# Kernel tuning notes

Measured on AMD Instinct MI355X. Metric: run time of the kernel, lower is better.

Reference implementation:

```python
import jax, jax.numpy as jnp
import numpy as np

N = 100000   # nodes (single 'paper' node type)
E = 1600000  # edges per relation
R = 3        # relation types
IN_DIM, HID_DIM, OUT_DIM = 128, 128, 64


def setup_inputs() -> dict:
    key = jax.random.key(0)
    ks = jax.random.split(key, 5)
    x = jax.random.normal(ks[0], (N, IN_DIM), dtype=jnp.float32)
    edges = jax.random.randint(ks[1], (R, 2, E), 0, N, dtype=jnp.int32)  # [rel, (src,dst), E]
    W1 = jax.random.normal(ks[2], (R, IN_DIM, HID_DIM), dtype=jnp.float32) * 0.05
    b1 = jnp.zeros((R, HID_DIM), dtype=jnp.float32)
    W2 = jax.random.normal(ks[3], (R, HID_DIM, OUT_DIM), dtype=jnp.float32) * 0.05
    b2 = jnp.zeros((R, OUT_DIM), dtype=jnp.float32)
    return {"x": x, "edges": edges, "W1": W1, "b1": b1, "W2": W2, "b2": b2}


def _hetero_gcn_layer(x, edges, W, b):
    """Per-relation DGL GraphConv (norm='both') summed across relations.
    y = sum_r  D_in_r^{-1/2} A_r^T (D_out_r^{-1/2} x) W_r + b_r
    """
    n = x.shape[0]
    ones = jnp.ones((edges.shape[-1],), x.dtype)
    out = jnp.zeros((n, W.shape[-1]), x.dtype)
    for r in range(edges.shape[0]):  # small fixed relation count
        src, dst = edges[r, 0], edges[r, 1]
        deg_out = jnp.maximum(jax.ops.segment_sum(ones, src, num_segments=n), 1.0)
        deg_in = jnp.maximum(jax.ops.segment_sum(ones, dst, num_segments=n), 1.0)
        # apply weight before aggregation (linear, math-equivalent; smaller msgs when out<=in)
        m = (x * (deg_out ** -0.5)[:, None]) @ W[r]          # [N, out]
        agg = jax.ops.segment_sum(m[src], dst, num_segments=n)  # gather+scatter SpMM
        out = out + agg * (deg_in ** -0.5)[:, None] + b[r]
    return out


def reference(x, edges, W1, b1, W2, b2):
    h = jax.nn.relu(_hetero_gcn_layer(x, edges, W1, b1))
    return _hetero_gcn_layer(h, edges, W2, b2)
```

## Files before the change

kernel.cpp:

```cpp
#include <hip/hip_runtime.h>

#define NODES 100000
#define NEDGE 1600000
#define NREL  3
#define DIN   128
#define DHID  128
#define DOUT  64

#define NBUCK 782
#define CHUNK 6144
#define NBLK  261
#define SEGCAP 8192

typedef unsigned short ushort_t;
typedef __attribute__((ext_vector_type(8))) short bf16x8;
typedef __attribute__((ext_vector_type(4))) float f32x4;

__device__ __forceinline__ unsigned f2bf1(float f) {
    unsigned u = __float_as_uint(f);
    return (u + 0x7fffu + ((u >> 16) & 1u)) >> 16;
}

__device__ __forceinline__ void scan_nbuck(unsigned* hist, unsigned* loff,
                                           unsigned* wred, int tid) {
    const int lane = tid & 63, wid = tid >> 6;
    unsigned s4[4];
    unsigned tsum = 0;
    const int sbase = tid * 4;
#pragma unroll
    for (int j = 0; j < 4; j++) {
        const unsigned c = (sbase + j < NBUCK) ? hist[sbase + j] : 0u;
        s4[j] = tsum;
        tsum += c;
    }
    unsigned incl = tsum;
    for (int o = 1; o < 64; o <<= 1) {
        const unsigned t = __shfl_up(incl, o, 64);
        if (lane >= o) incl += t;
    }
    if (lane == 63) wred[wid] = incl;
    __syncthreads();
    if (tid == 0) {
        unsigned a = 0;
        for (int w = 0; w < 4; w++) { const unsigned t = wred[w]; wred[w] = a; a += t; }
    }
    __syncthreads();
    const unsigned texcl = wred[wid] + incl - tsum;
#pragma unroll
    for (int j = 0; j < 4; j++)
        if (sbase + j < NBUCK) loff[sbase + j] = texcl + s4[j];
    __syncthreads();
}

__global__ __launch_bounds__(256) void partition_dst_kernel(
    const int* __restrict__ edges, int* __restrict__ bcur,
    unsigned* __restrict__ inter32) {
    __shared__ unsigned hist[NBUCK];
    __shared__ unsigned loff[NBUCK];
    __shared__ unsigned resv[NBUCK];
    __shared__ unsigned sorted[CHUNK];
    __shared__ ushort_t bof[CHUNK];
    __shared__ unsigned wred[4];
    const int tid = threadIdx.x;
    const int r = blockIdx.y;
    const int e0 = blockIdx.x * CHUNK;
    const int e1 = min(e0 + CHUNK, NEDGE);
    const int len = e1 - e0;
    const int* __restrict__ src = edges + (size_t)r * 2 * NEDGE;
    const int* __restrict__ dst = src + NEDGE;

    for (int i = tid; i < NBUCK; i += 256) hist[i] = 0;
    __syncthreads();
    for (int e = e0 + tid; e < e1; e += 256)
        atomicAdd(&hist[dst[e] >> 7], 1u);
    __syncthreads();
    scan_nbuck(hist, loff, wred, tid);
    for (int i = tid; i < NBUCK; i += 256) {
        const unsigned c = hist[i];
        resv[i] = c ? (unsigned)atomicAdd(&bcur[i], (int)c) : 0u;
        hist[i] = 0;
    }
    __syncthreads();
    for (int e = e0 + tid; e < e1; e += 256) {
        const int d = dst[e];
        const int b = d >> 7;
        const unsigned rank = atomicAdd(&hist[b], 1u);
        const unsigned pos = loff[b] + rank;
        sorted[pos] = ((unsigned)(d & 127) << 19) | (unsigned)(r * NODES + src[e]);
        bof[pos] = (ushort_t)b;
    }
    __syncthreads();
    for (int i = tid; i < len; i += 256) {
        const int b = bof[i];
        inter32[(size_t)b * SEGCAP + resv[b] + ((unsigned)i - loff[b])] = sorted[i];
    }
}

__global__ __launch_bounds__(256) void partition_src_kernel(
    const int* __restrict__ edges, int* __restrict__ bcur,
    ushort_t* __restrict__ inter16) {
    __shared__ unsigned hist[NBUCK];
    __shared__ unsigned loff[NBUCK];
    __shared__ unsigned resv[NBUCK];
    __shared__ unsigned sorted[CHUNK];
    __shared__ unsigned wred[4];
    const int tid = threadIdx.x;
    const int r = blockIdx.y;
    const int e0 = blockIdx.x * CHUNK;
    const int e1 = min(e0 + CHUNK, NEDGE);
    const int len = e1 - e0;
    const int* __restrict__ src = edges + (size_t)r * 2 * NEDGE;

    for (int i = tid; i < NBUCK; i += 256) hist[i] = 0;
    __syncthreads();
    for (int e = e0 + tid; e < e1; e += 256)
        atomicAdd(&hist[src[e] >> 7], 1u);
    __syncthreads();
    scan_nbuck(hist, loff, wred, tid);
    for (int i = tid; i < NBUCK; i += 256) {
        const unsigned c = hist[i];
        resv[i] = c ? (unsigned)atomicAdd(&bcur[i], (int)c) : 0u;
        hist[i] = 0;
    }
    __syncthreads();
    for (int e = e0 + tid; e < e1; e += 256) {
        const int s = src[e];
        const int b = s >> 7;
        const unsigned rank = atomicAdd(&hist[b], 1u);
        sorted[loff[b] + rank] =
            ((unsigned)b << 9) | ((unsigned)r << 7) | (unsigned)(s & 127);
    }
    __syncthreads();
    for (int i = tid; i < len; i += 256) {
        const unsigned w = sorted[i];
        const int b = w >> 9;
        inter16[(size_t)b * SEGCAP + resv[b] + ((unsigned)i - loff[b])] =
            (ushort_t)(w & 0x1ffu);
    }
}

__global__ __launch_bounds__(1024) void bscan_kernel(
    const int* __restrict__ bcur, int* __restrict__ bucketBase) {
    __shared__ int wsum[16];
    const int tid = threadIdx.x, lane = tid & 63, wid = tid >> 6;
    const int v = (tid < NBUCK) ? bcur[tid] : 0;
    int incl = v;
    for (int off = 1; off < 64; off <<= 1) {
        const int t = __shfl_up(incl, off, 64);
        if (lane >= off) incl += t;
    }
    if (lane == 63) wsum[wid] = incl;
    __syncthreads();
    if (tid == 0) {
        int a = 0;
        for (int w = 0; w < 16; w++) { const int t = wsum[w]; wsum[w] = a; a += t; }
    }
    __syncthreads();
    const int excl = wsum[wid] + incl - v;
    if (tid <= NBUCK) bucketBase[tid] = excl;
}

__global__ __launch_bounds__(256) void build_deg_kernel(
    const ushort_t* __restrict__ inter16, const int* __restrict__ bcur2,
    float* __restrict__ rout) {
    __shared__ int degR[NREL][128];
    const int b = blockIdx.x;
    const int tid = threadIdx.x;
    const int len = bcur2[b];
    const ushort_t* __restrict__ seg = inter16 + (size_t)b * SEGCAP;
    for (int i = tid; i < NREL * 128; i += 256) ((int*)degR)[i] = 0;
    __syncthreads();
    for (int s = tid; s < len; s += 256) {
        const unsigned p = seg[s];
        atomicAdd(&degR[p >> 7][p & 127], 1);
    }
    __syncthreads();
    const int n0 = b << 7;
    if (tid < 128) {
        const int node = n0 + tid;
        if (node < NODES) {
#pragma unroll
            for (int r = 0; r < NREL; r++) {
                const int d = degR[r][tid];
                rout[r * NODES + node] = rsqrtf((float)(d ? d : 1));
            }
        }
    }
}

__global__ __launch_bounds__(256) void build_kernel(
    const unsigned* __restrict__ inter, const int* __restrict__ bucketBase,
    int* __restrict__ csr, int* __restrict__ rowptr, unsigned* __restrict__ rel01,
    float* __restrict__ rin) {
    __shared__ int degR[NREL][128];
    __shared__ int rp[129];
    __shared__ int cur3[NREL][128];
    __shared__ int csr_lds[SEGCAP];
    const int b = blockIdx.x;
    const int tid = threadIdx.x;
    const int n0 = b << 7;
    const int nn = min(128, NODES - n0);
    const int s0 = bucketBase[b], s1 = bucketBase[b + 1];
    const int len = s1 - s0;
    const unsigned* __restrict__ seg = inter + (size_t)b * SEGCAP;
    for (int i = tid; i < NREL * 128; i += 256) ((int*)degR)[i] = 0;
    __syncthreads();
    for (int s = tid; s < len; s += 256) {
        const unsigned w = seg[s];
        const int dl = w >> 19;
        const int p = (int)(w & 0x7FFFFu);
        const int rel = p < NODES ? 0 : (p < 2 * NODES ? 1 : 2);
        atomicAdd(&degR[rel][dl], 1);
    }
    __syncthreads();
    if (tid == 0) {
        int a = 0;
        for (int i = 0; i < 128; i++) {
            rp[i] = a;
            a += degR[0][i] + degR[1][i] + degR[2][i];
        }
        rp[128] = a;
    }
    __syncthreads();
    if (tid < 128) {
        const int c0 = rp[tid];
        cur3[0][tid] = c0;
        cur3[1][tid] = c0 + degR[0][tid];
        cur3[2][tid] = c0 + degR[0][tid] + degR[1][tid];
    }
    if (tid < nn) {
        const int node = n0 + tid;
        rowptr[node] = s0 + rp[tid];
        rel01[node] = (unsigned)degR[0][tid] | ((unsigned)degR[1][tid] << 16);
#pragma unroll
        for (int r = 0; r < NREL; r++) {
            const int d = degR[r][tid];
            rin[r * NODES + node] = rsqrtf((float)(d ? d : 1));
        }
    }
    if (b == NBUCK - 1 && tid == 0) rowptr[NODES] = s1;
    __syncthreads();
    for (int s = tid; s < len; s += 256) {
        const unsigned w = seg[s];
        const int dl = w >> 19;
        const int p = (int)(w & 0x7FFFFu);
        const int rel = p < NODES ? 0 : (p < 2 * NODES ? 1 : 2);
        const int srcn = p - rel * NODES;
        const int slot = atomicAdd(&cur3[rel][dl], 1);
        csr_lds[slot] = srcn;
    }
    __syncthreads();
    for (int i = tid; i < len; i += 256) csr[s0 + i] = csr_lds[i];
}

__global__ __launch_bounds__(256) void tobf_kernel(const float* __restrict__ x,
                                                   ushort_t* __restrict__ xb) {
    const size_t i = ((size_t)blockIdx.x * 256 + threadIdx.x) * 8;
    const float4 a = *(const float4*)(x + i);
    const float4 b = *(const float4*)(x + i + 4);
    uint4 p;
    p.x = f2bf1(a.x) | (f2bf1(a.y) << 16);
    p.y = f2bf1(a.z) | (f2bf1(a.w) << 16);
    p.z = f2bf1(b.x) | (f2bf1(b.y) << 16);
    p.w = f2bf1(b.z) | (f2bf1(b.w) << 16);
    *(uint4*)(xb + i) = p;
}

template <int ODIM>
__global__ __launch_bounds__(256) void mfma_gemm(
    const ushort_t* __restrict__ A, const float* __restrict__ rout_all,
    const float* __restrict__ W_all, ushort_t* __restrict__ m_all) {
    constexpr int PAD = DIN + 8;
    constexpr int NT = ODIM / 16;
    __shared__ ushort_t Al[64 * PAD];
    __shared__ ushort_t Wt[ODIM * PAD];
    const int tid = threadIdx.x;
    const int rel = blockIdx.y;
    const int row0 = blockIdx.x * 64;
    const float* __restrict__ rout = rout_all + (size_t)rel * NODES;
    const float* __restrict__ W = W_all + (size_t)rel * DIN * ODIM;
    ushort_t* __restrict__ mout = m_all + (size_t)rel * NODES * ODIM;

    for (int idx = tid * 8; idx < 64 * DIN; idx += 2048) {
        const int rr = idx >> 7;
        const int kk = idx & 127;
        const int row = row0 + rr;
        uint4 p = make_uint4(0u, 0u, 0u, 0u);
        if (row < NODES) p = *(const uint4*)(A + (size_t)row * DIN + kk);
        *(uint4*)(Al + rr * PAD + kk) = p;
    }
    for (int idx = tid; idx < ODIM * (DIN / 8); idx += 256) {
        const int c = idx % ODIM;
        const int kh = idx / ODIM;
        unsigned pk[4];
#pragma unroll
        for (int j = 0; j < 4; j++) {
            const float lo = W[(size_t)(kh * 8 + 2 * j) * ODIM + c];
            const float hi = W[(size_t)(kh * 8 + 2 * j + 1) * ODIM + c];
            pk[j] = f2bf1(lo) | (f2bf1(hi) << 16);
        }
        *(uint4*)(Wt + c * PAD + kh * 8) = *(const uint4*)pk;
    }
    __syncthreads();

    const int l = tid & 63;
    const int wv = tid >> 6;
    const int lr = l & 15;
    const int lg = l >> 4;
    f32x4 acc[NT];
#pragma unroll
    for (int j = 0; j < NT; j++) acc[j] = (f32x4){0.f, 0.f, 0.f, 0.f};

    const ushort_t* ap = Al + (wv * 16 + lr) * PAD + lg * 8;
    const ushort_t* bp = Wt + lr * PAD + lg * 8;
#pragma unroll
    for (int ks = 0; ks < DIN; ks += 32) {
        const bf16x8 af = *(const bf16x8*)(ap + ks);
#pragma unroll
        for (int j = 0; j < NT; j++) {
            const bf16x8 bfr = *(const bf16x8*)(bp + (size_t)j * 16 * PAD + ks);
            acc[j] = __builtin_amdgcn_mfma_f32_16x16x32_bf16(af, bfr, acc[j], 0, 0, 0);
        }
    }

    const int orow0 = row0 + wv * 16 + lg * 4;
#pragma unroll
    for (int r = 0; r < 4; r++) {
        const int row = orow0 + r;
        if (row < NODES) {
            const float sc = rout[row];
#pragma unroll
            for (int j = 0; j < NT; j++)
                mout[(size_t)row * ODIM + j * 16 + lr] =
                    (ushort_t)f2bf1(acc[j][r] * sc);
        }
    }
}

template <int ODIM, bool L1>
__global__ __launch_bounds__(256) void agg_kernel(
    const ushort_t* __restrict__ m_all, const int* __restrict__ rowptr,
    const unsigned* __restrict__ rel01, const int* __restrict__ csr,
    const float* __restrict__ rin, const float* __restrict__ bias,
    float* __restrict__ outf, ushort_t* __restrict__ outh) {
    constexpr int CPT = ODIM / 16;
    const int v = blockIdx.x * 16 + (threadIdx.x >> 4);
    const int colbase = (threadIdx.x & 15) * CPT;
    const int b = rowptr[v];
    const int e2 = rowptr[v + 1];
    const unsigned c01 = rel01[v];
    const int cnt0 = (int)(c01 & 0xffffu);
    const int cnt1 = (int)(c01 >> 16);

    float acc[CPT];
#pragma unroll
    for (int j = 0; j < CPT; j++) acc[j] = 0.f;

    const ushort_t* mr = m_all + colbase;
    int beg = b;
#pragma unroll
    for (int r = 0; r < NREL; r++) {
        const int end = (r == 0) ? b + cnt0 : (r == 1) ? b + cnt0 + cnt1 : e2;
        float s[CPT];
#pragma unroll
        for (int j = 0; j < CPT; j++) s[j] = 0.f;
#pragma unroll 4
        for (int i = beg; i < end; i++) {
            const unsigned off = (unsigned)csr[i] * ODIM;
            if constexpr (CPT == 8) {
                const uint4 p = *(const uint4*)(mr + off);
                s[0] += __uint_as_float(p.x << 16);
                s[1] += __uint_as_float(p.x & 0xffff0000u);
                s[2] += __uint_as_float(p.y << 16);
                s[3] += __uint_as_float(p.y & 0xffff0000u);
                s[4] += __uint_as_float(p.z << 16);
                s[5] += __uint_as_float(p.z & 0xffff0000u);
                s[6] += __uint_as_float(p.w << 16);
                s[7] += __uint_as_float(p.w & 0xffff0000u);
            } else {
                const uint2 p = *(const uint2*)(mr + off);
                s[0] += __uint_as_float(p.x << 16);
                s[1] += __uint_as_float(p.x & 0xffff0000u);
                s[2] += __uint_as_float(p.y << 16);
                s[3] += __uint_as_float(p.y & 0xffff0000u);
            }
        }
        const float sc = rin[r * NODES + v];
#pragma unroll
        for (int j = 0; j < CPT; j++) acc[j] = fmaf(s[j], sc, acc[j]);
        beg = end;
        mr += (size_t)NODES * ODIM;
    }

    if (L1) {
        unsigned pk[CPT / 2];
#pragma unroll
        for (int j = 0; j < CPT; j += 2) {
            const int c0 = colbase + j, c1 = colbase + j + 1;
            const float v0 = fmaxf(acc[j] + bias[c0] + bias[ODIM + c0] + bias[2 * ODIM + c0], 0.f);
            const float v1 = fmaxf(acc[j + 1] + bias[c1] + bias[ODIM + c1] + bias[2 * ODIM + c1], 0.f);
            pk[j / 2] = f2bf1(v0) | (f2bf1(v1) << 16);
        }
        *(uint4*)(outh + (size_t)v * ODIM + colbase) = *(const uint4*)pk;
    } else {
        float o[CPT];
#pragma unroll
        for (int j = 0; j < CPT; j++) {
            const int c = colbase + j;
            o[j] = acc[j] + bias[c] + bias[ODIM + c] + bias[2 * ODIM + c];
        }
        *(float4*)(outf + (size_t)v * ODIM + colbase) = *(const float4*)o;
    }
}

extern "C" void kernel_launch(void* const* d_in, const int* in_sizes, int n_in,
                              void* d_out, int out_size, void* d_ws, size_t ws_size,
                              hipStream_t stream) {
    const float* x  = (const float*)d_in[0];
    const int* edges = (const int*)d_in[1];
    const float* W1 = (const float*)d_in[2];
    const float* b1 = (const float*)d_in[3];
    const float* W2 = (const float*)d_in[4];
    const float* b2 = (const float*)d_in[5];
    float* out = (float*)d_out;

    char* ws = (char*)d_ws;
    size_t off = 0;
    auto alloc = [&](size_t bytes) {
        void* p = ws + off;
        off = (off + bytes + 255) & ~(size_t)255;
        return p;
    };
    float*    rout   = (float*)alloc((size_t)NREL * NODES * 4);
    float*    rin    = (float*)alloc((size_t)NREL * NODES * 4);
    int*      bcur   = (int*)alloc((size_t)2 * NBUCK * 4);
    int*      bcur2  = bcur + NBUCK;
    int*      bbase  = (int*)alloc((size_t)(NBUCK + 1) * 4);
    int*      rowptr = (int*)alloc((size_t)(NODES + 1) * 4);
    unsigned* rel01  = (unsigned*)alloc((size_t)NODES * 4);
    int*      csr    = (int*)alloc((size_t)NREL * NEDGE * 4);
    ushort_t* m_all  = (ushort_t*)alloc((size_t)NREL * NODES * DHID * 2);
    ushort_t* h      = (ushort_t*)alloc((size_t)NODES * DHID * 2);
    unsigned* inter  = (unsigned*)m_all;
    ushort_t* inter2 = (ushort_t*)((char*)m_all + (size_t)NBUCK * SEGCAP * 4);
    ushort_t* xb     = h;

    hipMemsetAsync(bcur, 0, (size_t)2 * NBUCK * 4, stream);
    partition_dst_kernel<<<dim3(NBLK, NREL), 256, 0, stream>>>(edges, bcur, inter);
    partition_src_kernel<<<dim3(NBLK, NREL), 256, 0, stream>>>(edges, bcur2, inter2);
    bscan_kernel<<<1, 1024, 0, stream>>>(bcur, bbase);
    build_deg_kernel<<<NBUCK, 256, 0, stream>>>(inter2, bcur2, rout);
    build_kernel<<<NBUCK, 256, 0, stream>>>(inter, bbase, csr, rowptr, rel01, rin);

    tobf_kernel<<<NODES * DIN / 2048, 256, 0, stream>>>(x, xb);

    mfma_gemm<DHID><<<dim3((NODES + 63) / 64, NREL), 256, 0, stream>>>(
        xb, rout, W1, m_all);
    agg_kernel<DHID, true><<<NODES / 16, 256, 0, stream>>>(
        m_all, rowptr, rel01, csr, rin, b1, nullptr, h);

    mfma_gemm<DOUT><<<dim3((NODES + 63) / 64, NREL), 256, 0, stream>>>(
        h, rout, W2, m_all);
    agg_kernel<DOUT, false><<<NODES / 16, 256, 0, stream>>>(
        m_all, rowptr, rel01, csr, rin, b2, out, nullptr);
}
```

Before: 504.4 us.

## Reorder layer one to aggregate features before applying relation weights

Layer one now aggregates first and transforms second. A new aggregation kernel gathers the shared bf16 input features directly, applies the per-source out-degree scale on each edge, and writes one normalized aggregate per relation. A fused GEMM then multiplies each relation's aggregate by its weight, accumulates across the three relations, adds the bias and applies ReLU. The aim is to gather from one shared feature array instead of three relation-specific transformed arrays, which should improve cache reuse and remove the bias and ReLU epilogue from the aggregation step. In exchange, every edge now also gathers one extra scale value, and the three aggregate arrays still have to be written out and read back.

```diff
diff --git a/kernel.cpp b/kernel.cpp
--- a/kernel.cpp
+++ b/kernel.cpp
@@ -266,151 +266,228 @@
     *(uint4*)(xb + i) = p;
 }
 
-template <int ODIM>
-__global__ __launch_bounds__(256) void mfma_gemm(
-    const ushort_t* __restrict__ A, const float* __restrict__ rout_all,
-    const float* __restrict__ W_all, ushort_t* __restrict__ m_all) {
-    constexpr int PAD = DIN + 8;
-    constexpr int NT = ODIM / 16;
-    __shared__ ushort_t Al[64 * PAD];
-    __shared__ ushort_t Wt[ODIM * PAD];
-    const int tid = threadIdx.x;
-    const int rel = blockIdx.y;
-    const int row0 = blockIdx.x * 64;
-    const float* __restrict__ rout = rout_all + (size_t)rel * NODES;
-    const float* __restrict__ W = W_all + (size_t)rel * DIN * ODIM;
-    ushort_t* __restrict__ mout = m_all + (size_t)rel * NODES * ODIM;
-
-    for (int idx = tid * 8; idx < 64 * DIN; idx += 2048) {
-        const int rr = idx >> 7;
-        const int kk = idx & 127;
-        const int row = row0 + rr;
-        uint4 p = make_uint4(0u, 0u, 0u, 0u);
-        if (row < NODES) p = *(const uint4*)(A + (size_t)row * DIN + kk);
-        *(uint4*)(Al + rr * PAD + kk) = p;
-    }
-    for (int idx = tid; idx < ODIM * (DIN / 8); idx += 256) {
-        const int c = idx % ODIM;
-        const int kh = idx / ODIM;
-        unsigned pk[4];
-#pragma unroll
-        for (int j = 0; j < 4; j++) {
-            const float lo = W[(size_t)(kh * 8 + 2 * j) * ODIM + c];
-            const float hi = W[(size_t)(kh * 8 + 2 * j + 1) * ODIM + c];
-            pk[j] = f2bf1(lo) | (f2bf1(hi) << 16);
-        }
-        *(uint4*)(Wt + c * PAD + kh * 8) = *(const uint4*)pk;
-    }
-    __syncthreads();
-
-    const int l = tid & 63;
-    const int wv = tid >> 6;
-    const int lr = l & 15;
-    const int lg = l >> 4;
-    f32x4 acc[NT];
-#pragma unroll
-    for (int j = 0; j < NT; j++) acc[j] = (f32x4){0.f, 0.f, 0.f, 0.f};
-
-    const ushort_t* ap = Al + (wv * 16 + lr) * PAD + lg * 8;
-    const ushort_t* bp = Wt + lr * PAD + lg * 8;
-#pragma unroll
-    for (int ks = 0; ks < DIN; ks += 32) {
-        const bf16x8 af = *(const bf16x8*)(ap + ks);
-#pragma unroll
-        for (int j = 0; j < NT; j++) {
-            const bf16x8 bfr = *(const bf16x8*)(bp + (size_t)j * 16 * PAD + ks);
-            acc[j] = __builtin_amdgcn_mfma_f32_16x16x32_bf16(af, bfr, acc[j], 0, 0, 0);
-        }
-    }
-
-    const int orow0 = row0 + wv * 16 + lg * 4;
-#pragma unroll
-    for (int r = 0; r < 4; r++) {
-        const int row = orow0 + r;
-        if (row < NODES) {
-            const float sc = rout[row];
-#pragma unroll
-            for (int j = 0; j < NT; j++)
-                mout[(size_t)row * ODIM + j * 16 + lr] =
-                    (ushort_t)f2bf1(acc[j][r] * sc);
-        }
-    }
-}
-
-template <int ODIM, bool L1>
-__global__ __launch_bounds__(256) void agg_kernel(
-    const ushort_t* __restrict__ m_all, const int* __restrict__ rowptr,
+__global__ __launch_bounds__(256) void agg1_kernel(
+    const ushort_t* __restrict__ xb, const int* __restrict__ rowptr,
     const unsigned* __restrict__ rel01, const int* __restrict__ csr,
-    const float* __restrict__ rin, const float* __restrict__ bias,
-    float* __restrict__ outf, ushort_t* __restrict__ outh) {
-    constexpr int CPT = ODIM / 16;
+    const float* __restrict__ rout, const float* __restrict__ rin,
+    ushort_t* __restrict__ agg_all) {
     const int v = blockIdx.x * 16 + (threadIdx.x >> 4);
-    const int colbase = (threadIdx.x & 15) * CPT;
+    const int colbase = (threadIdx.x & 15) * 8;
     const int b = rowptr[v];
     const int e2 = rowptr[v + 1];
     const unsigned c01 = rel01[v];
     const int cnt0 = (int)(c01 & 0xffffu);
     const int cnt1 = (int)(c01 >> 16);
-
-    float acc[CPT];
-#pragma unroll
-    for (int j = 0; j < CPT; j++) acc[j] = 0.f;
+    const ushort_t* __restrict__ mr = xb + colbase;
+
+    int beg = b;
+#pragma unroll
+    for (int r = 0; r < NREL; r++) {
+        const int end = (r == 0) ? b + cnt0 : (r == 1) ? b + cnt0 + cnt1 : e2;
+        float s[8];
+#pragma unroll
+        for (int j = 0; j < 8; j++) s[j] = 0.f;
+        const float* __restrict__ rout_r = rout + (size_t)r * NODES;
+#pragma unroll 2
+        for (int i = beg; i < end; i++) {
+            const int sidx = csr[i];
+            const uint4 p = *(const uint4*)(mr + (unsigned)sidx * DIN);
+            const float w = rout_r[sidx];
+            s[0] = fmaf(w, __uint_as_float(p.x << 16), s[0]);
+            s[1] = fmaf(w, __uint_as_float(p.x & 0xffff0000u), s[1]);
+            s[2] = fmaf(w, __uint_as_float(p.y << 16), s[2]);
+            s[3] = fmaf(w, __uint_as_float(p.y & 0xffff0000u), s[3]);
+            s[4] = fmaf(w, __uint_as_float(p.z << 16), s[4]);
+            s[5] = fmaf(w, __uint_as_float(p.z & 0xffff0000u), s[5]);
+            s[6] = fmaf(w, __uint_as_float(p.w << 16), s[6]);
+            s[7] = fmaf(w, __uint_as_float(p.w & 0xffff0000u), s[7]);
+        }
+        const float sc = rin[(size_t)r * NODES + v];
+        unsigned pk[4];
+#pragma unroll
+        for (int j = 0; j < 8; j += 2)
+            pk[j / 2] = f2bf1(s[j] * sc) | (f2bf1(s[j + 1] * sc) << 16);
+        *(uint4*)(agg_all + ((size_t)r * NODES + v) * DIN + colbase) =
+            *(const uint4*)pk;
+        beg = end;
+    }
+}
+
+__global__ __launch_bounds__(256) void gemm1_kernel(
+    const ushort_t* __restrict__ agg_all, const float* __restrict__ W_all,
+    const float* __restrict__ b1, ushort_t* __restrict__ hout) {
+    constexpr int PAD = DIN + 8;
+    constexpr int NT = DHID / 16;
+    __shared__ ushort_t Al[64 * PAD];
+    __shared__ ushort_t Wt[DHID * PAD];
+    const int tid = threadIdx.x;
+    const int row0 = blockIdx.x * 64;
+    const int l = tid & 63, wv = tid >> 6, lr = l & 15, lg = l >> 4;
+    f32x4 acc[NT];
+#pragma unroll
+    for (int j = 0; j < NT; j++) acc[j] = (f32x4){0.f, 0.f, 0.f, 0.f};
+
+    for (int r = 0; r < NREL; r++) {
+        __syncthreads();
+        for (int idx = tid * 8; idx < 64 * DIN; idx += 2048) {
+            const int rr = idx >> 7, kk = idx & 127;
+            const int row = row0 + rr;
+            uint4 p = make_uint4(0u, 0u, 0u, 0u);
+            if (row < NODES)
+                p = *(const uint4*)(agg_all + ((size_t)r * NODES + row) * DIN + kk);
+            *(uint4*)(Al + rr * PAD + kk) = p;
+        }
+        const float* __restrict__ W = W_all + (size_t)r * DIN * DHID;
+        for (int idx = tid; idx < DHID * (DIN / 8); idx += 256) {
+            const int c = idx % DHID, kh = idx / DHID;
+            unsigned pk[4];
+#pragma unroll
+            for (int j = 0; j < 4; j++) {
+                const float lo = W[(size_t)(kh * 8 + 2 * j) * DHID + c];
+                const float hi = W[(size_t)(kh * 8 + 2 * j + 1) * DHID + c];
+                pk[j] = f2bf1(lo) | (f2bf1(hi) << 16);
+            }
+            *(uint4*)(Wt + c * PAD + kh * 8) = *(const uint4*)pk;
+        }
+        __syncthreads();
+        const ushort_t* ap = Al + (wv * 16 + lr) * PAD + lg * 8;
+        const ushort_t* bp = Wt + lr * PAD + lg * 8;
+#pragma unroll
+        for (int ks = 0; ks < DIN; ks += 32) {
+            const bf16x8 af = *(const bf16x8*)(ap + ks);
+#pragma unroll
+            for (int j = 0; j < NT; j++) {
+                const bf16x8 bfr = *(const bf16x8*)(bp + (size_t)j * 16 * PAD + ks);
+                acc[j] = __builtin_amdgcn_mfma_f32_16x16x32_bf16(af, bfr, acc[j], 0, 0, 0);
+            }
+        }
+    }
+    const int orow0 = row0 + wv * 16 + lg * 4;
+#pragma unroll
+    for (int rg = 0; rg < 4; rg++) {
+        const int row = orow0 + rg;
+        if (row < NODES) {
+#pragma unroll
+            for (int j = 0; j < NT; j++) {
+                const int c = j * 16 + lr;
+                const float bs = b1[c] + b1[DHID + c] + b1[2 * DHID + c];
+                hout[(size_t)row * DHID + c] =
+                    (ushort_t)f2bf1(fmaxf(acc[j][rg] + bs, 0.f));
+            }
+        }
+    }
+}
+
+__global__ __launch_bounds__(256) void gemm2_kernel(
+    const ushort_t* __restrict__ A, const float* __restrict__ rout_all,
+    const float* __restrict__ W_all, ushort_t* __restrict__ m_all) {
+    constexpr int PAD = DIN + 8;
+    constexpr int NT = DOUT / 16;
+    __shared__ ushort_t Al[64 * PAD];
+    __shared__ ushort_t Wt[DOUT * PAD];
+    const int tid = threadIdx.x;
+    const int rel = blockIdx.y;
+    const int row0 = blockIdx.x * 64;
+    const float* __restrict__ rout = rout_all + (size_t)rel * NODES;
+    const float* __restrict__ W = W_all + (size_t)rel * DIN * DOUT;
+    ushort_t* __restrict__ mout = m_all + (size_t)rel * NODES * DOUT;
+
+    for (int idx = tid * 8; idx < 64 * DIN; idx += 2048) {
+        const int rr = idx >> 7, kk = idx & 127;
+        const int row = row0 + rr;
+        uint4 p = make_uint4(0u, 0u, 0u, 0u);
+        if (row < NODES) p = *(const uint4*)(A + (size_t)row * DIN + kk);
+        *(uint4*)(Al + rr * PAD + kk) = p;
+    }
+    for (int idx = tid; idx < DOUT * (DIN / 8); idx += 256) {
+        const int c = idx % DOUT, kh = idx / DOUT;
+        unsigned pk[4];
+#pragma unroll
+        for (int j = 0; j < 4; j++) {
+            const float lo = W[(size_t)(kh * 8 + 2 * j) * DOUT + c];
+            const float hi = W[(size_t)(kh * 8 + 2 * j + 1) * DOUT + c];
+            pk[j] = f2bf1(lo) | (f2bf1(hi) << 16);
+        }
+        *(uint4*)(Wt + c * PAD + kh * 8) = *(const uint4*)pk;
+    }
+    __syncthreads();
+
+    const int l = tid & 63, wv = tid >> 6, lr = l & 15, lg = l >> 4;
+    f32x4 acc[NT];
+#pragma unroll
+    for (int j = 0; j < NT; j++) acc[j] = (f32x4){0.f, 0.f, 0.f, 0.f};
+    const ushort_t* ap = Al + (wv * 16 + lr) * PAD + lg * 8;
+    const ushort_t* bp = Wt + lr * PAD + lg * 8;
+#pragma unroll
+    for (int ks = 0; ks < DIN; ks += 32) {
+        const bf16x8 af = *(const bf16x8*)(ap + ks);
+#pragma unroll
+        for (int j = 0; j < NT; j++) {
+            const bf16x8 bfr = *(const bf16x8*)(bp + (size_t)j * 16 * PAD + ks);
+            acc[j] = __builtin_amdgcn_mfma_f32_16x16x32_bf16(af, bfr, acc[j], 0, 0, 0);
+        }
+    }
+    const int orow0 = row0 + wv * 16 + lg * 4;
+#pragma unroll
+    for (int rg = 0; rg < 4; rg++) {
+        const int row = orow0 + rg;
+        if (row < NODES) {
+            const float sc = rout[row];
+#pragma unroll
+            for (int j = 0; j < NT; j++)
+                mout[(size_t)row * DOUT + j * 16 + lr] =
+                    (ushort_t)f2bf1(acc[j][rg] * sc);
+        }
+    }
+}
+
+__global__ __launch_bounds__(256) void agg2_kernel(
+    const ushort_t* __restrict__ m_all, const int* __restrict__ rowptr,
+    const unsigned* __restrict__ rel01, const int* __restrict__ csr,
+    const float* __restrict__ rin, const float* __restrict__ bias,
+    float* __restrict__ outf) {
+    const int v = blockIdx.x * 16 + (threadIdx.x >> 4);
+    const int colbase = (threadIdx.x & 15) * 4;
+    const int b = rowptr[v];
+    const int e2 = rowptr[v + 1];
+    const unsigned c01 = rel01[v];
+    const int cnt0 = (int)(c01 & 0xffffu);
+    const int cnt1 = (int)(c01 >> 16);
+
+    float acc[4];
+#pragma unroll
+    for (int j = 0; j < 4; j++) acc[j] = 0.f;
 
     const ushort_t* mr = m_all + colbase;
     int beg = b;
 #pragma unroll
     for (int r = 0; r < NREL; r++) {
         const int end = (r == 0) ? b + cnt0 : (r == 1) ? b + cnt0 + cnt1 : e2;
-        float s[CPT];
-#pragma unroll
-        for (int j = 0; j < CPT; j++) s[j] = 0.f;
+        float s[4];
+#pragma unroll
+        for (int j = 0; j < 4; j++) s[j] = 0.f;
 #pragma unroll 4
         for (int i = beg; i < end; i++) {
-            const unsigned off = (unsigned)csr[i] * ODIM;
-            if constexpr (CPT == 8) {
-                const uint4 p = *(const uint4*)(mr + off);
-                s[0] += __uint_as_float(p.x << 16);
-                s[1] += __uint_as_float(p.x & 0xffff0000u);
-                s[2] += __uint_as_float(p.y << 16);
-                s[3] += __uint_as_float(p.y & 0xffff0000u);
-                s[4] += __uint_as_float(p.z << 16);
-                s[5] += __uint_as_float(p.z & 0xffff0000u);
-                s[6] += __uint_as_float(p.w << 16);
-                s[7] += __uint_as_float(p.w & 0xffff0000u);
-            } else {
-                const uint2 p = *(const uint2*)(mr + off);
-                s[0] += __uint_as_float(p.x << 16);
-                s[1] += __uint_as_float(p.x & 0xffff0000u);
-                s[2] += __uint_as_float(p.y << 16);
-                s[3] += __uint_as_float(p.y & 0xffff0000u);
-            }
+            const unsigned off = (unsigned)csr[i] * DOUT;
+            const uint2 p = *(const uint2*)(mr + off);
+            s[0] += __uint_as_float(p.x << 16);
+            s[1] += __uint_as_float(p.x & 0xffff0000u);
+            s[2] += __uint_as_float(p.y << 16);
+            s[3] += __uint_as_float(p.y & 0xffff0000u);
         }
         const float sc = rin[r * NODES + v];
 #pragma unroll
-        for (int j = 0; j < CPT; j++) acc[j] = fmaf(s[j], sc, acc[j]);
+        for (int j = 0; j < 4; j++) acc[j] = fmaf(s[j], sc, acc[j]);
         beg = end;
-        mr += (size_t)NODES * ODIM;
-    }
-
-    if (L1) {
-        unsigned pk[CPT / 2];
-#pragma unroll
-        for (int j = 0; j < CPT; j += 2) {
-            const int c0 = colbase + j, c1 = colbase + j + 1;
-            const float v0 = fmaxf(acc[j] + bias[c0] + bias[ODIM + c0] + bias[2 * ODIM + c0], 0.f);
-            const float v1 = fmaxf(acc[j + 1] + bias[c1] + bias[ODIM + c1] + bias[2 * ODIM + c1], 0.f);
-            pk[j / 2] = f2bf1(v0) | (f2bf1(v1) << 16);
-        }
-        *(uint4*)(outh + (size_t)v * ODIM + colbase) = *(const uint4*)pk;
-    } else {
-        float o[CPT];
-#pragma unroll
-        for (int j = 0; j < CPT; j++) {
-            const int c = colbase + j;
-            o[j] = acc[j] + bias[c] + bias[ODIM + c] + bias[2 * ODIM + c];
-        }
-        *(float4*)(outf + (size_t)v * ODIM + colbase) = *(const float4*)o;
-    }
+        mr += (size_t)NODES * DOUT;
+    }
+    float o[4];
+#pragma unroll
+    for (int j = 0; j < 4; j++) {
+        const int c = colbase + j;
+        o[j] = acc[j] + bias[c] + bias[DOUT + c] + bias[2 * DOUT + c];
+    }
+    *(float4*)(outf + (size_t)v * DOUT + colbase) = *(const float4*)o;
 }
 
 extern "C" void kernel_launch(void* const* d_in, const int* in_sizes, int n_in,
@@ -454,13 +531,12 @@
 
     tobf_kernel<<<NODES * DIN / 2048, 256, 0, stream>>>(x, xb);
 
-    mfma_gemm<DHID><<<dim3((NODES + 63) / 64, NREL), 256, 0, stream>>>(
-        xb, rout, W1, m_all);
-    agg_kernel<DHID, true><<<NODES / 16, 256, 0, stream>>>(
-        m_all, rowptr, rel01, csr, rin, b1, nullptr, h);
-
-    mfma_gemm<DOUT><<<dim3((NODES + 63) / 64, NREL), 256, 0, stream>>>(
+    agg1_kernel<<<NODES / 16, 256, 0, stream>>>(
+        xb, rowptr, rel01, csr, rout, rin, m_all);
+    gemm1_kernel<<<(NODES + 63) / 64, 256, 0, stream>>>(m_all, W1, b1, h);
+
+    gemm2_kernel<<<dim3((NODES + 63) / 64, NREL), 256, 0, stream>>>(
         h, rout, W2, m_all);
-    agg_kernel<DOUT, false><<<NODES / 16, 256, 0, stream>>>(
-        m_all, rowptr, rel01, csr, rin, b2, out, nullptr);
-}
+    agg2_kernel<<<NODES / 16, 256, 0, stream>>>(
+        m_all, rowptr, rel01, csr, rin, b2, out);
+}
```

Measured after the change: 531.8 us. 1.05x slower.

## Fuse partition passes, degree build, bf16 cast and per-relation GEMMs into fewer kernels

Applied to the files above, without the earlier changes.

Merges the dst and src partition kernels into one launch and folds the out-degree computation into build_kernel. It also removes the separate fp32-to-bf16 conversion kernel by converting x inside the GEMM tile load. The GEMM now loops over all three relations within one block, so the A tile is loaded once per block rather than once per relation. The aim is fewer launches and less repeated reading of x/h, at the cost of serial per-relation work inside each block, fewer blocks in the GEMM grid, and reloading and re-converting W three times per block.

```diff
diff --git a/kernel.cpp b/kernel.cpp
--- a/kernel.cpp
+++ b/kernel.cpp
@@ -52,9 +52,10 @@
     __syncthreads();
 }
 
-__global__ __launch_bounds__(256) void partition_dst_kernel(
-    const int* __restrict__ edges, int* __restrict__ bcur,
-    unsigned* __restrict__ inter32) {
+__global__ __launch_bounds__(256) void partition_kernel(
+    const int* __restrict__ edges, int* __restrict__ bcurD,
+    int* __restrict__ bcurS, unsigned* __restrict__ inter32,
+    ushort_t* __restrict__ inter16) {
     __shared__ unsigned hist[NBUCK];
     __shared__ unsigned loff[NBUCK];
     __shared__ unsigned resv[NBUCK];
@@ -77,7 +78,7 @@
     scan_nbuck(hist, loff, wred, tid);
     for (int i = tid; i < NBUCK; i += 256) {
         const unsigned c = hist[i];
-        resv[i] = c ? (unsigned)atomicAdd(&bcur[i], (int)c) : 0u;
+        resv[i] = c ? (unsigned)atomicAdd(&bcurD[i], (int)c) : 0u;
         hist[i] = 0;
     }
     __syncthreads();
@@ -94,22 +95,7 @@
         const int b = bof[i];
         inter32[(size_t)b * SEGCAP + resv[b] + ((unsigned)i - loff[b])] = sorted[i];
     }
-}
-
-__global__ __launch_bounds__(256) void partition_src_kernel(
-    const int* __restrict__ edges, int* __restrict__ bcur,
-    ushort_t* __restrict__ inter16) {
-    __shared__ unsigned hist[NBUCK];
-    __shared__ unsigned loff[NBUCK];
-    __shared__ unsigned resv[NBUCK];
-    __shared__ unsigned sorted[CHUNK];
-    __shared__ unsigned wred[4];
-    const int tid = threadIdx.x;
-    const int r = blockIdx.y;
-    const int e0 = blockIdx.x * CHUNK;
-    const int e1 = min(e0 + CHUNK, NEDGE);
-    const int len = e1 - e0;
-    const int* __restrict__ src = edges + (size_t)r * 2 * NEDGE;
+    __syncthreads();
 
     for (int i = tid; i < NBUCK; i += 256) hist[i] = 0;
     __syncthreads();
@@ -119,7 +105,7 @@
     scan_nbuck(hist, loff, wred, tid);
     for (int i = tid; i < NBUCK; i += 256) {
         const unsigned c = hist[i];
-        resv[i] = c ? (unsigned)atomicAdd(&bcur[i], (int)c) : 0u;
+        resv[i] = c ? (unsigned)atomicAdd(&bcurS[i], (int)c) : 0u;
         hist[i] = 0;
     }
     __syncthreads();
@@ -160,38 +146,11 @@
     if (tid <= NBUCK) bucketBase[tid] = excl;
 }
 
-__global__ __launch_bounds__(256) void build_deg_kernel(
-    const ushort_t* __restrict__ inter16, const int* __restrict__ bcur2,
-    float* __restrict__ rout) {
-    __shared__ int degR[NREL][128];
-    const int b = blockIdx.x;
-    const int tid = threadIdx.x;
-    const int len = bcur2[b];
-    const ushort_t* __restrict__ seg = inter16 + (size_t)b * SEGCAP;
-    for (int i = tid; i < NREL * 128; i += 256) ((int*)degR)[i] = 0;
-    __syncthreads();
-    for (int s = tid; s < len; s += 256) {
-        const unsigned p = seg[s];
-        atomicAdd(&degR[p >> 7][p & 127], 1);
-    }
-    __syncthreads();
-    const int n0 = b << 7;
-    if (tid < 128) {
-        const int node = n0 + tid;
-        if (node < NODES) {
-#pragma unroll
-            for (int r = 0; r < NREL; r++) {
-                const int d = degR[r][tid];
-                rout[r * NODES + node] = rsqrtf((float)(d ? d : 1));
-            }
-        }
-    }
-}
-
 __global__ __launch_bounds__(256) void build_kernel(
-    const unsigned* __restrict__ inter, const int* __restrict__ bucketBase,
+    const unsigned* __restrict__ inter32, const int* __restrict__ bucketBase,
+    const ushort_t* __restrict__ inter16, const int* __restrict__ bcurS,
     int* __restrict__ csr, int* __restrict__ rowptr, unsigned* __restrict__ rel01,
-    float* __restrict__ rin) {
+    float* __restrict__ rin, float* __restrict__ rout) {
     __shared__ int degR[NREL][128];
     __shared__ int rp[129];
     __shared__ int cur3[NREL][128];
@@ -202,7 +161,8 @@
     const int nn = min(128, NODES - n0);
     const int s0 = bucketBase[b], s1 = bucketBase[b + 1];
     const int len = s1 - s0;
-    const unsigned* __restrict__ seg = inter + (size_t)b * SEGCAP;
+    const unsigned* __restrict__ seg = inter32 + (size_t)b * SEGCAP;
+
     for (int i = tid; i < NREL * 128; i += 256) ((int*)degR)[i] = 0;
     __syncthreads();
     for (int s = tid; s < len; s += 256) {
@@ -251,88 +211,103 @@
     }
     __syncthreads();
     for (int i = tid; i < len; i += 256) csr[s0 + i] = csr_lds[i];
-}
-
-__global__ __launch_bounds__(256) void tobf_kernel(const float* __restrict__ x,
-                                                   ushort_t* __restrict__ xb) {
-    const size_t i = ((size_t)blockIdx.x * 256 + threadIdx.x) * 8;
-    const float4 a = *(const float4*)(x + i);
-    const float4 b = *(const float4*)(x + i + 4);
-    uint4 p;
-    p.x = f2bf1(a.x) | (f2bf1(a.y) << 16);
-    p.y = f2bf1(a.z) | (f2bf1(a.w) << 16);
-    p.z = f2bf1(b.x) | (f2bf1(b.y) << 16);
-    p.w = f2bf1(b.z) | (f2bf1(b.w) << 16);
-    *(uint4*)(xb + i) = p;
-}
-
-template <int ODIM>
-__global__ __launch_bounds__(256) void mfma_gemm(
-    const ushort_t* __restrict__ A, const float* __restrict__ rout_all,
+
+    __syncthreads();
+    for (int i = tid; i < NREL * 128; i += 256) ((int*)degR)[i] = 0;
+    __syncthreads();
+    const int len2 = bcurS[b];
+    const ushort_t* __restrict__ seg16 = inter16 + (size_t)b * SEGCAP;
+    for (int s = tid; s < len2; s += 256) {
+        const unsigned p = seg16[s];
+        atomicAdd(&degR[p >> 7][p & 127], 1);
+    }
+    __syncthreads();
+    if (tid < nn) {
+        const int node = n0 + tid;
+#pragma unroll
+        for (int r = 0; r < NREL; r++) {
+            const int d = degR[r][tid];
+            rout[r * NODES + node] = rsqrtf((float)(d ? d : 1));
+        }
+    }
+}
+
+template <int ODIM, bool IN_F32>
+__global__ __launch_bounds__(256) void gemm_fused(
+    const void* __restrict__ A, const float* __restrict__ rout_all,
     const float* __restrict__ W_all, ushort_t* __restrict__ m_all) {
     constexpr int PAD = DIN + 8;
     constexpr int NT = ODIM / 16;
     __shared__ ushort_t Al[64 * PAD];
     __shared__ ushort_t Wt[ODIM * PAD];
     const int tid = threadIdx.x;
-    const int rel = blockIdx.y;
     const int row0 = blockIdx.x * 64;
-    const float* __restrict__ rout = rout_all + (size_t)rel * NODES;
-    const float* __restrict__ W = W_all + (size_t)rel * DIN * ODIM;
-    ushort_t* __restrict__ mout = m_all + (size_t)rel * NODES * ODIM;
 
     for (int idx = tid * 8; idx < 64 * DIN; idx += 2048) {
-        const int rr = idx >> 7;
-        const int kk = idx & 127;
+        const int rr = idx >> 7, kk = idx & 127;
         const int row = row0 + rr;
         uint4 p = make_uint4(0u, 0u, 0u, 0u);
-        if (row < NODES) p = *(const uint4*)(A + (size_t)row * DIN + kk);
+        if (row < NODES) {
+            if (IN_F32) {
+                const float* Af = (const float*)A + (size_t)row * DIN + kk;
+                const float4 a = *(const float4*)Af;
+                const float4 b = *(const float4*)(Af + 4);
+                p.x = f2bf1(a.x) | (f2bf1(a.y) << 16);
+                p.y = f2bf1(a.z) | (f2bf1(a.w) << 16);
+                p.z = f2bf1(b.x) | (f2bf1(b.y) << 16);
+                p.w = f2bf1(b.z) | (f2bf1(b.w) << 16);
+            } else {
+                p = *(const uint4*)((const ushort_t*)A + (size_t)row * DIN + kk);
+            }
+        }
         *(uint4*)(Al + rr * PAD + kk) = p;
     }
-    for (int idx = tid; idx < ODIM * (DIN / 8); idx += 256) {
-        const int c = idx % ODIM;
-        const int kh = idx / ODIM;
-        unsigned pk[4];
-#pragma unroll
-        for (int j = 0; j < 4; j++) {
-            const float lo = W[(size_t)(kh * 8 + 2 * j) * ODIM + c];
-            const float hi = W[(size_t)(kh * 8 + 2 * j + 1) * ODIM + c];
-            pk[j] = f2bf1(lo) | (f2bf1(hi) << 16);
-        }
-        *(uint4*)(Wt + c * PAD + kh * 8) = *(const uint4*)pk;
-    }
-    __syncthreads();
-
-    const int l = tid & 63;
-    const int wv = tid >> 6;
-    const int lr = l & 15;
-    const int lg = l >> 4;
-    f32x4 acc[NT];
-#pragma unroll
-    for (int j = 0; j < NT; j++) acc[j] = (f32x4){0.f, 0.f, 0.f, 0.f};
-
-    const ushort_t* ap = Al + (wv * 16 + lr) * PAD + lg * 8;
-    const ushort_t* bp = Wt + lr * PAD + lg * 8;
-#pragma unroll
-    for (int ks = 0; ks < DIN; ks += 32) {
-        const bf16x8 af = *(const bf16x8*)(ap + ks);
-#pragma unroll
-        for (int j = 0; j < NT; j++) {
-            const bf16x8 bfr = *(const bf16x8*)(bp + (size_t)j * 16 * PAD + ks);
-            acc[j] = __builtin_amdgcn_mfma_f32_16x16x32_bf16(af, bfr, acc[j], 0, 0, 0);
-        }
-    }
-
-    const int orow0 = row0 + wv * 16 + lg * 4;
-#pragma unroll
-    for (int r = 0; r < 4; r++) {
-        const int row = orow0 + r;
-        if (row < NODES) {
-            const float sc = rout[row];
-#pragma unroll
-            for (int j = 0; j < NT; j++)
-                mout[(size_t)row * ODIM + j * 16 + lr] =
-                    (ushort_t)f2bf1(acc[j][r] * sc);
+
+    const int l = tid & 63, wv = tid >> 6, lr = l & 15, lg = l >> 4;
+    for (int r = 0; r < NREL; r++) {
+        __syncthreads();
+        const float* __restrict__ W = W_all + (size_t)r * DIN * ODIM;
+        for (int idx = tid; idx < ODIM * (DIN / 8); idx += 256) {
+            const int c = idx % ODIM, kh = idx / ODIM;
+            unsigned pk[4];
+#pragma unroll
+            for (int j = 0; j < 4; j++) {
+                const float lo = W[(size_t)(kh * 8 + 2 * j) * ODIM + c];
+                const float hi = W[(size_t)(kh * 8 + 2 * j + 1) * ODIM + c];
+                pk[j] = f2bf1(lo) | (f2bf1(hi) << 16);
+            }
+            *(uint4*)(Wt + c * PAD + kh * 8) = *(const uint4*)pk;
+        }
+        __syncthreads();
+
+        f32x4 acc[NT];
+#pragma unroll
+        for (int j = 0; j < NT; j++) acc[j] = (f32x4){0.f, 0.f, 0.f, 0.f};
+        const ushort_t* ap = Al + (wv * 16 + lr) * PAD + lg * 8;
+        const ushort_t* bp = Wt + lr * PAD + lg * 8;
+#pragma unroll
+        for (int ks = 0; ks < DIN; ks += 32) {
+            const bf16x8 af = *(const bf16x8*)(ap + ks);
+#pragma unroll
+            for (int j = 0; j < NT; j++) {
+                const bf16x8 bfr = *(const bf16x8*)(bp + (size_t)j * 16 * PAD + ks);
+                acc[j] = __builtin_amdgcn_mfma_f32_16x16x32_bf16(af, bfr, acc[j], 0, 0, 0);
+            }
+        }
+
+        const float* __restrict__ rout = rout_all + (size_t)r * NODES;
+        ushort_t* __restrict__ mout = m_all + (size_t)r * NODES * ODIM;
+        const int orow0 = row0 + wv * 16 + lg * 4;
+#pragma unroll
+        for (int rg = 0; rg < 4; rg++) {
+            const int row = orow0 + rg;
+            if (row < NODES) {
+                const float sc = rout[row];
+#pragma unroll
+                for (int j = 0; j < NT; j++)
+                    mout[(size_t)row * ODIM + j * 16 + lr] =
+                        (ushort_t)f2bf1(acc[j][rg] * sc);
+            }
         }
     }
 }
@@ -434,32 +409,29 @@
     float*    rout   = (float*)alloc((size_t)NREL * NODES * 4);
     float*    rin    = (float*)alloc((size_t)NREL * NODES * 4);
     int*      bcur   = (int*)alloc((size_t)2 * NBUCK * 4);
-    int*      bcur2  = bcur + NBUCK;
+    int*      bcurS  = bcur + NBUCK;
     int*      bbase  = (int*)alloc((size_t)(NBUCK + 1) * 4);
     int*      rowptr = (int*)alloc((size_t)(NODES + 1) * 4);
     unsigned* rel01  = (unsigned*)alloc((size_t)NODES * 4);
     int*      csr    = (int*)alloc((size_t)NREL * NEDGE * 4);
     ushort_t* m_all  = (ushort_t*)alloc((size_t)NREL * NODES * DHID * 2);
     ushort_t* h      = (ushort_t*)alloc((size_t)NODES * DHID * 2);
-    unsigned* inter  = (unsigned*)m_all;
-    ushort_t* inter2 = (ushort_t*)((char*)m_all + (size_t)NBUCK * SEGCAP * 4);
-    ushort_t* xb     = h;
+    unsigned* inter32 = (unsigned*)m_all;
+    ushort_t* inter16 = (ushort_t*)((char*)m_all + (size_t)NBUCK * SEGCAP * 4);
 
     hipMemsetAsync(bcur, 0, (size_t)2 * NBUCK * 4, stream);
-    partition_dst_kernel<<<dim3(NBLK, NREL), 256, 0, stream>>>(edges, bcur, inter);
-    partition_src_kernel<<<dim3(NBLK, NREL), 256, 0, stream>>>(edges, bcur2, inter2);
+    partition_kernel<<<dim3(NBLK, NREL), 256, 0, stream>>>(
+        edges, bcur, bcurS, inter32, inter16);
     bscan_kernel<<<1, 1024, 0, stream>>>(bcur, bbase);
-    build_deg_kernel<<<NBUCK, 256, 0, stream>>>(inter2, bcur2, rout);
-    build_kernel<<<NBUCK, 256, 0, stream>>>(inter, bbase, csr, rowptr, rel01, rin);
-
-    tobf_kernel<<<NODES * DIN / 2048, 256, 0, stream>>>(x, xb);
-
-    mfma_gemm<DHID><<<dim3((NODES + 63) / 64, NREL), 256, 0, stream>>>(
-        xb, rout, W1, m_all);
+    build_kernel<<<NBUCK, 256, 0, stream>>>(
+        inter32, bbase, inter16, bcurS, csr, rowptr, rel01, rin, rout);
+
+    gemm_fused<DHID, true><<<(NODES + 63) / 64, 256, 0, stream>>>(
+        x, rout, W1, m_all);
     agg_kernel<DHID, true><<<NODES / 16, 256, 0, stream>>>(
         m_all, rowptr, rel01, csr, rin, b1, nullptr, h);
 
-    mfma_gemm<DOUT><<<dim3((NODES + 63) / 64, NREL), 256, 0, stream>>>(
+    gemm_fused<DOUT, false><<<(NODES + 63) / 64, 256, 0, stream>>>(
         h, rout, W2, m_all);
     agg_kernel<DOUT, false><<<NODES / 16, 256, 0, stream>>>(
         m_all, rowptr, rel01, csr, rin, b2, out, nullptr);
```

New measurement: 479.7 us, median of 3. 1.05x faster.
